# Optimization experiments

Hardware: AMD Instinct MI355X
Metric: run time of the kernel (lower is better)

The kernel has to match this reference:

```python
import jax, jax.numpy as jnp
import numpy as np

HQ, HKV, D, BS = 128, 16, 128, 128  # q heads, kv heads, head dim, block size
ROPE_BASE = 10000.0


def rope(x):
    # x: (B, S, H, D); rotate-half RoPE with cos/sin tiled to full head dim
    d = x.shape[-1]
    inv_freq = 1.0 / (ROPE_BASE ** (jnp.arange(0, d, 2, dtype=jnp.float32) / d))  # (D/2,)
    pos = jnp.arange(x.shape[1], dtype=jnp.float32)
    ang = pos[:, None] * inv_freq[None, :]                      # (S, D/2)
    cos = jnp.tile(jnp.cos(ang), (1, 2))[None, :, None, :]      # (1, S, 1, D)
    sin = jnp.tile(jnp.sin(ang), (1, 2))[None, :, None, :]
    x1, x2 = x[..., : d // 2], x[..., d // 2 :]
    x_rot = jnp.concatenate([-x2, x1], axis=-1)
    return x * cos + x_rot * sin


def setup_inputs() -> dict:
    key = jax.random.key(0)
    ks = jax.random.split(key, 5)
    s = 0.02
    E, B, S = 8192, 2, 2048
    return {
        "x": jax.random.normal(ks[0], (B, S, E), jnp.float32),
        "Wq": jax.random.normal(ks[1], (E, HQ * D), jnp.float32) * s,
        "bq": jnp.zeros((HQ * D,), jnp.float32),
        "Wk": jax.random.normal(ks[2], (E, HKV * D), jnp.float32) * s,
        "bk": jnp.zeros((HKV * D,), jnp.float32),
        "Wv": jax.random.normal(ks[3], (E, HKV * D), jnp.float32) * s,
        "bv": jnp.zeros((HKV * D,), jnp.float32),
        "Wo": jax.random.normal(ks[4], (HQ * D, E), jnp.float32) * s,
        "bo": jnp.zeros((E,), jnp.float32),
    }


def reference(x, Wq, bq, Wk, bk, Wv, bv, Wo, bo):
    B, S, E = x.shape
    G = HQ // HKV  # q heads per kv head (GQA group size) = 8
    nb = S // BS   # number of non-overlapping attention blocks

    q = (x @ Wq + bq).reshape(B, S, HQ, D)
    k = (x @ Wk + bk).reshape(B, S, HKV, D)
    v = (x @ Wv + bv).reshape(B, S, HKV, D)
    q = rope(q)
    k = rope(k)

    # Block-diagonal attention: queries only attend within their own block.
    qb = q.reshape(B, nb, BS, HKV, G, D)   # group consecutive q heads per kv head
    kb = k.reshape(B, nb, BS, HKV, D)
    vb = v.reshape(B, nb, BS, HKV, D)

    scale = 1.0 / jnp.sqrt(jnp.float32(D))
    logits = jnp.einsum('bnqhgd,bnkhd->bnhgqk', qb, kb) * scale  # (B,nb,HKV,G,BS,BS)
    attn = jax.nn.softmax(logits, axis=-1)
    ob = jnp.einsum('bnhgqk,bnkhd->bnqhgd', attn, vb)            # (B,nb,BS,HKV,G,D)
    attn_out = ob.reshape(B, S, HQ * D)

    out = attn_out @ Wo + bo
    return out, k, v
```

## Files before the change

### kernel.cpp

```cpp
#include <hip/hip_runtime.h>

typedef __attribute__((ext_vector_type(8))) short bf16x8;
typedef __attribute__((ext_vector_type(8))) unsigned short u16x8;
typedef __attribute__((ext_vector_type(4))) float f32x4;

__device__ __forceinline__ unsigned short f2bf(float f){
    unsigned int u = __builtin_bit_cast(unsigned int, f);
    u += 0x7fffu + ((u >> 16) & 1u);
    return (unsigned short)(u >> 16);
}
__device__ __forceinline__ float bf2f(unsigned short h){
    unsigned int u = ((unsigned int)h) << 16;
    return __builtin_bit_cast(float, u);
}
__device__ __forceinline__ f32x4 mfma16(bf16x8 a, bf16x8 b, f32x4 c){
    return __builtin_amdgcn_mfma_f32_16x16x32_bf16(a, b, c, 0, 0, 0);
}
__device__ __forceinline__ void gl16(const unsigned short* g, unsigned short* l){
    __builtin_amdgcn_global_load_lds(
        (const __attribute__((address_space(1))) unsigned int*)g,
        (__attribute__((address_space(3))) unsigned int*)l, 16, 0, 0);
}
#define BAR() asm volatile("s_barrier" ::: "memory")

__global__ __launch_bounds__(256) void cvt_x_kernel(const float* __restrict__ x,
                                                    unsigned short* __restrict__ xb){
    size_t i = ((size_t)blockIdx.x * 256 + threadIdx.x) * 4;
    float4 f = *(const float4*)(x + i);
    ushort4 o;
    o.x = f2bf(f.x); o.y = f2bf(f.y); o.z = f2bf(f.z); o.w = f2bf(f.w);
    *(ushort4*)(xb + i) = o;
}

__global__ __launch_bounds__(256) void tr_kernel(const float* __restrict__ W, int ldn, int col0, int K,
                                                 unsigned short* __restrict__ Wt){
    __shared__ unsigned short T[64][66];
    const int t  = threadIdx.x;
    const int k0 = blockIdx.x << 6;
    const int n0 = blockIdx.y << 6;
    #pragma unroll
    for (int i = 0; i < 4; ++i){
        const int idx = i*256 + t;
        const int r   = idx >> 4;
        const int c4  = idx & 15;
        float4 v = *(const float4*)(W + (size_t)(k0 + r)*ldn + col0 + n0 + c4*4);
        T[r][c4*4+0] = f2bf(v.x); T[r][c4*4+1] = f2bf(v.y);
        T[r][c4*4+2] = f2bf(v.z); T[r][c4*4+3] = f2bf(v.w);
    }
    __syncthreads();
    const int n  = t >> 2;
    const int ks = (t & 3) * 16;
    u16x8 o0, o1;
    #pragma unroll
    for (int j = 0; j < 8; ++j){ o0[j] = T[ks+j][n]; o1[j] = T[ks+8+j][n]; }
    unsigned short* dst = Wt + (size_t)(n0 + n)*K + k0 + ks;
    *(u16x8*)dst       = o0;
    *(u16x8*)(dst + 8) = o1;
}

#define READ_A(MH) do { _Pragma("unroll") for (int m_=0;m_<4;++m_){           \
    const int ro_ = (wm*128 + (MH)*64 + m_*16 + llo)*64;                      \
    Af[m_][0] = *(const bf16x8*)&S[curA + ro_ + rdc0];                        \
    Af[m_][1] = *(const bf16x8*)&S[curA + ro_ + rdc1]; } } while(0)

#define READ_B(NH) do { _Pragma("unroll") for (int n_=0;n_<2;++n_){           \
    const int ro_ = (wn*64 + (NH)*32 + n_*16 + llo)*64;                       \
    Bf[(NH)*2+n_][0] = *(const bf16x8*)&S[curB + ro_ + rdc0];                 \
    Bf[(NH)*2+n_][1] = *(const bf16x8*)&S[curB + ro_ + rdc1]; } } while(0)

#define QUADRANT(AB, NH) do {                                                 \
    __builtin_amdgcn_s_setprio(1);                                            \
    _Pragma("unroll") for (int m_=0;m_<4;++m_){                               \
      _Pragma("unroll") for (int n_=0;n_<2;++n_){                             \
        f32x4 &a_ = acc[(AB)+m_][(NH)*2+n_];                                  \
        a_ = mfma16(Af[m_][0], Bf[(NH)*2+n_][0], a_);                         \
        a_ = mfma16(Af[m_][1], Bf[(NH)*2+n_][1], a_);                         \
    } }                                                                       \
    __builtin_amdgcn_s_setprio(0);                                            \
} while(0)

template<int EPI>
__global__ __launch_bounds__(512, 2) void gemm256_kernel(
    const unsigned short* __restrict__ A, int K,
    const unsigned short* __restrict__ Bt, int n_off,
    const float* __restrict__ bq, const float* __restrict__ bk_,
    const float* __restrict__ bv_, const float* __restrict__ bo_,
    unsigned short* __restrict__ q_ws,
    float* __restrict__ k_out, float* __restrict__ v_out,
    unsigned short* __restrict__ v_ws,
    float* __restrict__ outp)
{
    __shared__ unsigned short S[65536];

    const int t    = threadIdx.x;
    const int lane = t & 63;
    const int wid  = t >> 6;
    const int wm   = wid >> 2, wn = wid & 3;
    const int llo  = lane & 15, lhi = lane >> 4;
    const int wslot = wid * 512;
    const int rdswz = (((llo >> 1) & 1) << 4) | ((llo & 1) << 5);
    const int rdc0  = (lhi * 8) ^ rdswz;
    const int rdc1  = rdc0 ^ 32;

    const int nwg = gridDim.x;
    const int qx  = nwg >> 3;
    const int nb  = (blockIdx.x & 7) * qx + (blockIdx.x >> 3);
    const int tm  = nb & 15;
    const int tn  = nb >> 4;
    const int brow  = tm * 256;
    const int nbase = tn * 256;
    const int gcol0 = n_off + nbase;

    const int srow = t >> 3;
    const int scol = ((t & 7) * 8) ^ (((t >> 4) & 1) << 4) ^ (((t >> 3) & 1) << 5);
    const unsigned short* pA0 = A  + (size_t)(brow  + srow)*K + scol;
    const unsigned short* pA1 = pA0 + (size_t)128*K;
    const unsigned short* pB0 = Bt + (size_t)(nbase + srow)*K + scol;
    const unsigned short* pB1 = pB0 + (size_t)128*K;

    auto stage = [&](const unsigned short* gb, int ktt, int ldsoff){
        const unsigned short* g0 = gb + (size_t)ktt * 64;
        gl16(g0,                 &S[ldsoff + wslot]);
        gl16(g0 + (size_t)64*K,  &S[ldsoff + wslot + 4096]);
    };

    const f32x4 zero = {0.f,0.f,0.f,0.f};
    f32x4 acc[8][4];
    #pragma unroll
    for (int i = 0; i < 8; ++i)
        #pragma unroll
        for (int j = 0; j < 4; ++j) acc[i][j] = zero;

    bf16x8 Af[4][2], Bf[4][2];
    const int NT = K >> 6;

    stage(pB0, 0, 16384);
    stage(pA0, 0, 0);
    stage(pA1, 0, 8192);
    stage(pB1, 0, 24576);
    stage(pB0, 1, 32768 + 16384);
    stage(pA0, 1, 32768);
    asm volatile("s_waitcnt vmcnt(4)" ::: "memory");
    BAR();

    for (int kt = 0; kt < NT; ++kt){
        const int cur = kt & 1, nxt = cur ^ 1;
        const int curA = cur * 32768, curB = curA + 16384;
        const int nxtA = nxt * 32768, nxtB = nxtA + 16384;

        READ_A(0); READ_B(0);
        if (kt + 1 < NT) stage(pA1, kt + 1, nxtA + 8192);
        BAR();
        QUADRANT(0, 0);
        BAR();

        READ_B(1);
        if (kt + 1 < NT) stage(pB1, kt + 1, nxtB + 8192);
        BAR();
        QUADRANT(0, 1);
        BAR();

        READ_A(1);
        if (kt + 2 < NT) stage(pB0, kt + 2, curB);
        BAR();
        QUADRANT(4, 1);
        BAR();

        if (kt + 2 < NT){
            stage(pA0, kt + 2, curA);
            asm volatile("s_waitcnt vmcnt(4)" ::: "memory");
        } else {
            asm volatile("s_waitcnt vmcnt(0)" ::: "memory");
        }
        BAR();
        QUADRANT(4, 0);
        BAR();
    }

    #pragma unroll
    for (int mi = 0; mi < 8; ++mi){
        #pragma unroll
        for (int ni = 0; ni < 4; ++ni){
            const int col = gcol0 + wn*64 + ni*16 + llo;
            int region;
            if (EPI == 1)          region = 3;
            else if (col < 16384)  region = 0;
            else if (col < 18432)  region = 1;
            else                   region = 2;
            float bias;
            if (region == 3)      bias = bo_[col];
            else if (region == 0) bias = bq[col];
            else if (region == 1) bias = bk_[col - 16384];
            else                  bias = bv_[col - 18432];
            const int row0 = brow + wm*128 + mi*16 + lhi*4;
            #pragma unroll
            for (int r = 0; r < 4; ++r){
                const float val = acc[mi][ni][r] + bias;
                const size_t rr = (size_t)(row0 + r);
                if (region == 3){
                    outp[rr * 8192 + col] = val;
                } else if (region == 0){
                    q_ws[rr * 16384 + col] = f2bf(val);
                } else if (region == 1){
                    k_out[rr * 2048 + (col - 16384)] = val;
                } else {
                    v_out[rr * 2048 + (col - 18432)] = val;
                    v_ws[rr * 2048 + (col - 18432)]  = f2bf(val);
                }
            }
        }
    }
}

__global__ __launch_bounds__(256) void rope_q_kernel(unsigned short* __restrict__ q){
    const size_t idx = (size_t)blockIdx.x * 256 + threadIdx.x;
    const int i = (int)(idx & 63);
    const int h = (int)((idx >> 6) & 127);
    const int r = (int)(idx >> 13);
    const int s = r & 2047;
    const float inv = exp2f(-(float)i * 0.20762050593046014f);
    float c, sn;
    sincosf((float)s * inv, &sn, &c);
    unsigned short* p = q + (size_t)r * 16384 + h * 128 + i;
    const float v1 = bf2f(p[0]);
    const float v2 = bf2f(p[64]);
    p[0]  = f2bf(v1 * c - v2 * sn);
    p[64] = f2bf(v2 * c + v1 * sn);
}

__global__ __launch_bounds__(256) void rope_k_kernel(float* __restrict__ kio,
                                                     unsigned short* __restrict__ kws){
    const size_t idx = (size_t)blockIdx.x * 256 + threadIdx.x;
    const int i = (int)(idx & 63);
    const int h = (int)((idx >> 6) & 15);
    const int r = (int)(idx >> 10);
    const int s = r & 2047;
    const float inv = exp2f(-(float)i * 0.20762050593046014f);
    float c, sn;
    sincosf((float)s * inv, &sn, &c);
    float* p = kio + (size_t)r * 2048 + h * 128 + i;
    const float v1 = p[0], v2 = p[64];
    const float o1 = v1 * c - v2 * sn;
    const float o2 = v2 * c + v1 * sn;
    p[0] = o1; p[64] = o2;
    unsigned short* pw = kws + (size_t)r * 2048 + h * 128 + i;
    pw[0]  = f2bf(o1);
    pw[64] = f2bf(o2);
}

__global__ __launch_bounds__(256) void attn_kernel(
    const unsigned short* __restrict__ q,
    const unsigned short* __restrict__ kbf,
    const unsigned short* __restrict__ vbf,
    unsigned short* __restrict__ ao)
{
    __shared__ unsigned short KV[128][136];
    __shared__ unsigned short Pls[4][16][136];

    const int t    = threadIdx.x;
    const int lane = t & 63;
    const int wid  = t >> 6;
    const int llo  = lane & 15, lhi = lane >> 4;

    const int bid = blockIdx.x;
    const int qh  = bid & 1;
    const int g   = (bid >> 1) & 7;
    const int hkv = (bid >> 4) & 15;
    const int blk = (bid >> 8) & 15;
    const int b   = bid >> 12;

    const int h     = hkv * 8 + g;
    const int sbase = b * 2048 + blk * 128;
    const int qbase = sbase + qh * 64 + wid * 16;

    {
        const int row = t >> 1;
        const int d0  = (t & 1) * 64;
        const unsigned short* src = kbf + (size_t)(sbase + row) * 2048 + hkv * 128 + d0;
        #pragma unroll
        for (int i2 = 0; i2 < 8; ++i2)
            *(int4*)&KV[row][d0 + i2*8] = *(const int4*)(src + i2*8);
    }

    bf16x8 qf[4];
    {
        const unsigned short* qp = q + (size_t)(qbase + llo) * 16384 + h * 128 + lhi * 8;
        #pragma unroll
        for (int kc = 0; kc < 4; ++kc)
            qf[kc] = *(const bf16x8*)(qp + kc * 32);
    }

    __syncthreads();

    const f32x4 zero = {0.f,0.f,0.f,0.f};
    f32x4 sc[8];
    #pragma unroll
    for (int ni = 0; ni < 8; ++ni) sc[ni] = zero;
    #pragma unroll
    for (int kc = 0; kc < 4; ++kc){
        #pragma unroll
        for (int ni = 0; ni < 8; ++ni){
            bf16x8 kf = *(const bf16x8*)&KV[ni*16 + llo][kc*32 + lhi*8];
            sc[ni] = mfma16(qf[kc], kf, sc[ni]);
        }
    }

    const float scale = 0.08838834764831845f;
    #pragma unroll
    for (int r = 0; r < 4; ++r){
        float m = sc[0][r];
        #pragma unroll
        for (int ni = 1; ni < 8; ++ni) m = fmaxf(m, sc[ni][r]);
        #pragma unroll
        for (int off = 1; off < 16; off <<= 1) m = fmaxf(m, __shfl_xor(m, off));
        float sum = 0.f;
        #pragma unroll
        for (int ni = 0; ni < 8; ++ni){
            const float p = __expf((sc[ni][r] - m) * scale);
            sc[ni][r] = p; sum += p;
        }
        #pragma unroll
        for (int off = 1; off < 16; off <<= 1) sum += __shfl_xor(sum, off);
        const float rs = 1.f / sum;
        #pragma unroll
        for (int ni = 0; ni < 8; ++ni) sc[ni][r] *= rs;
    }

    #pragma unroll
    for (int ni = 0; ni < 8; ++ni)
        #pragma unroll
        for (int r = 0; r < 4; ++r)
            Pls[wid][lhi*4 + r][ni*16 + llo] = f2bf(sc[ni][r]);

    __syncthreads();

    {
        const int d  = t & 127;
        const int j0 = (t >> 7) * 64;
        const unsigned short* vs = vbf + (size_t)sbase * 2048 + hkv * 128 + d;
        #pragma unroll
        for (int jj = 0; jj < 64; jj += 8){
            u16x8 pk;
            #pragma unroll
            for (int e = 0; e < 8; ++e)
                pk[e] = vs[(size_t)(j0 + jj + e) * 2048];
            *(u16x8*)&KV[d][j0 + jj] = pk;
        }
    }

    __syncthreads();

    f32x4 oc[8];
    #pragma unroll
    for (int ni = 0; ni < 8; ++ni) oc[ni] = zero;
    #pragma unroll
    for (int kc = 0; kc < 4; ++kc){
        bf16x8 pf = *(const bf16x8*)&Pls[wid][llo][kc*32 + lhi*8];
        #pragma unroll
        for (int ni = 0; ni < 8; ++ni){
            bf16x8 vf = *(const bf16x8*)&KV[ni*16 + llo][kc*32 + lhi*8];
            oc[ni] = mfma16(pf, vf, oc[ni]);
        }
    }

    #pragma unroll
    for (int ni = 0; ni < 8; ++ni){
        #pragma unroll
        for (int r = 0; r < 4; ++r){
            const size_t row = (size_t)(qbase + lhi*4 + r);
            ao[row * 16384 + h*128 + ni*16 + llo] = f2bf(oc[ni][r]);
        }
    }
}

extern "C" void kernel_launch(void* const* d_in, const int* in_sizes, int n_in,
                              void* d_out, int out_size, void* d_ws, size_t ws_size,
                              hipStream_t stream)
{
    const float* x  = (const float*)d_in[0];
    const float* Wq = (const float*)d_in[1];
    const float* bq = (const float*)d_in[2];
    const float* Wk = (const float*)d_in[3];
    const float* bk = (const float*)d_in[4];
    const float* Wv = (const float*)d_in[5];
    const float* bv = (const float*)d_in[6];
    const float* Wo = (const float*)d_in[7];
    const float* bo = (const float*)d_in[8];

    float* outp  = (float*)d_out;
    float* k_out = outp + (size_t)33554432;
    float* v_out = outp + (size_t)41943040;

    char* w = (char*)d_ws;
    unsigned short* xb  = (unsigned short*)(w);
    unsigned short* kb2 = (unsigned short*)(w + 67108864ull);
    unsigned short* vb2 = (unsigned short*)(w + 83886080ull);
    unsigned short* qb  = (unsigned short*)(w + 100663296ull);
    unsigned short* Wt  = (unsigned short*)(w + 234881024ull);

    cvt_x_kernel<<<32768, 256, 0, stream>>>(x, xb);

    for (int c = 0; c < 4; ++c){
        tr_kernel<<<dim3(128, 64), 256, 0, stream>>>(Wq, 16384, c*4096, 8192, Wt);
        gemm256_kernel<0><<<256, 512, 0, stream>>>(xb, 8192, Wt, c*4096, bq, bk, bv, nullptr,
                                                   qb, k_out, v_out, vb2, nullptr);
    }
    tr_kernel<<<dim3(128, 32), 256, 0, stream>>>(Wk, 2048, 0, 8192, Wt);
    tr_kernel<<<dim3(128, 32), 256, 0, stream>>>(Wv, 2048, 0, 8192, Wt + (size_t)2048*8192);
    gemm256_kernel<0><<<256, 512, 0, stream>>>(xb, 8192, Wt, 16384, bq, bk, bv, nullptr,
                                               qb, k_out, v_out, vb2, nullptr);

    rope_q_kernel<<<131072, 256, 0, stream>>>(qb);
    rope_k_kernel<<<16384, 256, 0, stream>>>(k_out, kb2);
    attn_kernel<<<8192, 256, 0, stream>>>(qb, kb2, vb2, qb);

    for (int hh = 0; hh < 2; ++hh){
        tr_kernel<<<dim3(256, 64), 256, 0, stream>>>(Wo, 8192, hh*4096, 16384, Wt);
        gemm256_kernel<1><<<256, 512, 0, stream>>>(qb, 16384, Wt, hh*4096, nullptr, nullptr, nullptr, bo,
                                                   nullptr, nullptr, nullptr, nullptr, outp);
    }
}
```

Before: 2.907 ms.

## Prefetch next k-tile fragments during last quadrant and unroll loop by two

Restructures the GEMM main loop so each LDS fragment read is issued one phase ahead of the MFMA quadrant that consumes it. The next k-tile's A0/B0 fragments are read during the final quadrant of the current tile. The loop is unrolled by two with ping-pong B0 register buffers so buffer offsets become compile-time constants. This targets exposed LDS-read latency before MFMA bursts, at the cost of more VGPRs, which may hurt occupancy at launch bounds (512,2). It assumes NT is even.

After: 9.047 ms. 3.11x slower.

```diff
diff --git a/kernel.cpp b/kernel.cpp
--- a/kernel.cpp
+++ b/kernel.cpp
@@ -58,25 +58,56 @@
     *(u16x8*)(dst + 8) = o1;
 }
 
-#define READ_A(MH) do { _Pragma("unroll") for (int m_=0;m_<4;++m_){           \
+#define RD_A(dst, MH, BASE) do { _Pragma("unroll") for (int m_=0;m_<4;++m_){  \
     const int ro_ = (wm*128 + (MH)*64 + m_*16 + llo)*64;                      \
-    Af[m_][0] = *(const bf16x8*)&S[curA + ro_ + rdc0];                        \
-    Af[m_][1] = *(const bf16x8*)&S[curA + ro_ + rdc1]; } } while(0)
-
-#define READ_B(NH) do { _Pragma("unroll") for (int n_=0;n_<2;++n_){           \
+    dst[m_][0] = *(const bf16x8*)&S[(BASE) + ro_ + rdc0];                     \
+    dst[m_][1] = *(const bf16x8*)&S[(BASE) + ro_ + rdc1]; } } while(0)
+
+#define RD_B(dst, NH, BASE) do { _Pragma("unroll") for (int n_=0;n_<2;++n_){  \
     const int ro_ = (wn*64 + (NH)*32 + n_*16 + llo)*64;                       \
-    Bf[(NH)*2+n_][0] = *(const bf16x8*)&S[curB + ro_ + rdc0];                 \
-    Bf[(NH)*2+n_][1] = *(const bf16x8*)&S[curB + ro_ + rdc1]; } } while(0)
-
-#define QUADRANT(AB, NH) do {                                                 \
+    dst[n_][0] = *(const bf16x8*)&S[(BASE) + ro_ + rdc0];                     \
+    dst[n_][1] = *(const bf16x8*)&S[(BASE) + ro_ + rdc1]; } } while(0)
+
+#define QUAD(Asrc, Bsrc, AB, ACOL) do {                                       \
     __builtin_amdgcn_s_setprio(1);                                            \
     _Pragma("unroll") for (int m_=0;m_<4;++m_){                               \
       _Pragma("unroll") for (int n_=0;n_<2;++n_){                             \
-        f32x4 &a_ = acc[(AB)+m_][(NH)*2+n_];                                  \
-        a_ = mfma16(Af[m_][0], Bf[(NH)*2+n_][0], a_);                         \
-        a_ = mfma16(Af[m_][1], Bf[(NH)*2+n_][1], a_);                         \
+        f32x4 &a_ = acc[(AB)+m_][(ACOL)+n_];                                  \
+        a_ = mfma16(Asrc[m_][0], Bsrc[n_][0], a_);                            \
+        a_ = mfma16(Asrc[m_][1], Bsrc[n_][1], a_);                            \
     } }                                                                       \
     __builtin_amdgcn_s_setprio(0);                                            \
+} while(0)
+
+#define KT_BODY(KT, CA, CB, NA, NB, B0U, B0N) do {                            \
+                              \
+    RD_B(B1f, 1, CB);                                                         \
+    if ((KT) + 1 < NT) stage(pA1, (KT)+1, (NA)+8192);                         \
+    BAR();                                                                    \
+    QUAD(A0f, B0U, 0, 0);                                                     \
+    BAR();                                                                    \
+                              \
+    RD_A(A1f, 1, CA);                                                         \
+    if ((KT) + 1 < NT) stage(pB1, (KT)+1, (NB)+8192);                         \
+    BAR();                                                                    \
+    QUAD(A0f, B1f, 0, 2);                                                     \
+    BAR();                                                                    \
+         \
+    if ((KT) + 2 < NT) stage(pB0, (KT)+2, (CB));                              \
+    BAR();                                                                    \
+    QUAD(A1f, B1f, 4, 2);                                                     \
+    BAR();                                                                    \
+     \
+    if ((KT) + 2 < NT){                                                       \
+        stage(pA0, (KT)+2, (CA));                                             \
+        asm volatile("s_waitcnt vmcnt(4)" ::: "memory");                      \
+    } else {                                                                  \
+        asm volatile("s_waitcnt vmcnt(0)" ::: "memory");                      \
+    }                                                                         \
+    BAR();                                                                    \
+    if ((KT) + 1 < NT){ RD_A(A0f, 0, NA); RD_B(B0N, 0, NB); }                 \
+    QUAD(A1f, B0U, 4, 0);                                                     \
+    BAR();                                                                    \
 } while(0)
 
 template<int EPI>
@@ -131,7 +162,7 @@
         #pragma unroll
         for (int j = 0; j < 4; ++j) acc[i][j] = zero;
 
-    bf16x8 Af[4][2], Bf[4][2];
+    bf16x8 A0f[4][2], A1f[4][2], B1f[2][2], B0a[2][2], B0b[2][2];
     const int NT = K >> 6;
 
     stage(pB0, 0, 16384);
@@ -142,39 +173,12 @@
     stage(pA0, 1, 32768);
     asm volatile("s_waitcnt vmcnt(4)" ::: "memory");
     BAR();
-
-    for (int kt = 0; kt < NT; ++kt){
-        const int cur = kt & 1, nxt = cur ^ 1;
-        const int curA = cur * 32768, curB = curA + 16384;
-        const int nxtA = nxt * 32768, nxtB = nxtA + 16384;
-
-        READ_A(0); READ_B(0);
-        if (kt + 1 < NT) stage(pA1, kt + 1, nxtA + 8192);
-        BAR();
-        QUADRANT(0, 0);
-        BAR();
-
-        READ_B(1);
-        if (kt + 1 < NT) stage(pB1, kt + 1, nxtB + 8192);
-        BAR();
-        QUADRANT(0, 1);
-        BAR();
-
-        READ_A(1);
-        if (kt + 2 < NT) stage(pB0, kt + 2, curB);
-        BAR();
-        QUADRANT(4, 1);
-        BAR();
-
-        if (kt + 2 < NT){
-            stage(pA0, kt + 2, curA);
-            asm volatile("s_waitcnt vmcnt(4)" ::: "memory");
-        } else {
-            asm volatile("s_waitcnt vmcnt(0)" ::: "memory");
-        }
-        BAR();
-        QUADRANT(4, 0);
-        BAR();
+    RD_A(A0f, 0, 0);
+    RD_B(B0a, 0, 16384);
+
+    for (int kt = 0; kt < NT; kt += 2){
+        KT_BODY(kt,     0,     16384, 32768, 49152, B0a, B0b);
+        KT_BODY(kt + 1, 32768, 49152, 0,     16384, B0b, B0a);
     }
 
     #pragma unroll
```
